# Kernel tuning notes

Hardware: AMD Instinct MI355X
Metric: run time of the kernel (lower is better)

## Reference

```python
import jax, jax.numpy as jnp
import numpy as np

B, S, IN_DIM, OUT_DIM = 16, 1024, 1024, 1024
NEG_SLOPE = 0.01  # torch F.leaky_relu default


def setup_inputs() -> dict:
    key = jax.random.key(0)
    ks = jax.random.split(key, 10)
    sc_in = 1.0 / np.sqrt(IN_DIM)
    sc_out = 1.0 / np.sqrt(OUT_DIM)
    return {
        "xs": jax.random.normal(ks[0], (B, S, IN_DIM), dtype=jnp.float32),
        "mask": jax.random.randint(ks[1], (B, S), 0, 2, dtype=jnp.int32),
        "Wk": jax.random.uniform(ks[2], (OUT_DIM, IN_DIM), jnp.float32, -sc_in, sc_in),
        "bk": jax.random.uniform(ks[3], (OUT_DIM,), jnp.float32, -sc_in, sc_in),
        "Wq": jax.random.uniform(ks[4], (OUT_DIM, IN_DIM), jnp.float32, -sc_in, sc_in),
        "bq": jax.random.uniform(ks[5], (OUT_DIM,), jnp.float32, -sc_in, sc_in),
        "Wv": jax.random.uniform(ks[6], (OUT_DIM, IN_DIM), jnp.float32, -sc_in, sc_in),
        "bv": jax.random.uniform(ks[7], (OUT_DIM,), jnp.float32, -sc_in, sc_in),
        "Wlin": jax.random.uniform(ks[8], (OUT_DIM, OUT_DIM), jnp.float32, -sc_out, sc_out),
        "blin": jax.random.uniform(ks[9], (OUT_DIM,), jnp.float32, -sc_out, sc_out),
    }


def reference(xs, mask, Wk, bk, Wq, bq, Wv, bv, Wlin, blin):
    # projections: torch Linear is x @ W.T + b
    K = jnp.einsum('bsi,oi->bso', xs, Wk) + bk  # [B,S,D]
    Q = jnp.einsum('bsi,oi->bso', xs, Wq) + bq  # [B,S,D]
    V = jnp.einsum('bsi,oi->bso', xs, Wv) + bv  # [B,S,D]
    # qk[b,s,e] = sum_d K[b,s,d] * Q[b,e,d]
    qk = jnp.einsum('bsd,bed->bse', K, Q) / xs.shape[-1]
    # mask.repeat(1,S).view(B,S,S) => element [b,i,j] = mask[b,j] (column/key mask)
    qk = jnp.where(mask[:, None, :].astype(bool), qk, -jnp.inf)
    a = jax.nn.softmax(qk, axis=-1)  # [B,S,S]
    # faithful to einsum('bij,bik->bik'): sum a over last axis, scale V elementwise
    attn = jnp.sum(a, axis=-1, keepdims=True) * V  # [B,S,D]
    out = jnp.einsum('bsd,od->bso', attn, Wlin) + blin
    return jnp.where(out >= 0, out, NEG_SLOPE * out)
```

## Files before the change

### kernel.cpp

```cpp
#include <hip/hip_runtime.h>
#include <hip/hip_bf16.h>
#include <stdint.h>


#define M_TOT 16384
#define KDIM  1024
#define NDIM  1024
#define NKT   16

typedef __attribute__((ext_vector_type(8))) short bf16x8;
typedef __attribute__((ext_vector_type(4))) float f32x4;
typedef __attribute__((ext_vector_type(4))) unsigned short u16x4;
typedef __attribute__((ext_vector_type(8))) unsigned short u16x8;

static __device__ __forceinline__ unsigned short f2bf(float f) {
    union { float f; unsigned int u; } v; v.f = f;
    unsigned int u = v.u;
    return (unsigned short)((u + 0x7fffu + ((u >> 16) & 1u)) >> 16);
}

static __device__ __forceinline__ u16x8 pack8(float4 a, float4 b) {
    u16x8 p = { f2bf(a.x), f2bf(a.y), f2bf(a.z), f2bf(a.w),
                f2bf(b.x), f2bf(b.y), f2bf(b.z), f2bf(b.w) };
    return p;
}

static __device__ __forceinline__ void gload16(const void* g, void* l) {
    __builtin_amdgcn_global_load_lds(
        (__attribute__((address_space(1))) void*)(g),
        (__attribute__((address_space(3))) void*)(l), 16, 0, 0);
}

static __device__ __forceinline__ int swz128(int p) {
    return p ^ (((p >> 7) & 7) << 4);
}

__global__ __launch_bounds__(256) void prep0_kernel(
    const float* __restrict__ Wv, const float* __restrict__ Wlin,
    const float* __restrict__ bv, const float* __restrict__ blin,
    unsigned short* __restrict__ Wvt, unsigned short* __restrict__ Wlb,
    float* __restrict__ bcomb) {
    __shared__ float Tl[64 * 65];
    const int bid = blockIdx.x;
    const int t = threadIdx.x;

    if (bid < 256) {
        const int dt = bid >> 4;
        const int it = bid & 15;
        const int r = t >> 2;
        const int c0 = (t & 3) * 16;
        #pragma unroll
        for (int u = 0; u < 4; ++u) {
            float4 v = *(const float4*)&Wv[((size_t)(dt * 64 + r)) * NDIM + it * 64 + c0 + 4 * u];
            Tl[r * 65 + c0 + 4 * u + 0] = v.x;
            Tl[r * 65 + c0 + 4 * u + 1] = v.y;
            Tl[r * 65 + c0 + 4 * u + 2] = v.z;
            Tl[r * 65 + c0 + 4 * u + 3] = v.w;
        }
        __syncthreads();
        const int i = t >> 2;
        const int dq = (t & 3) * 16;
        float v[16];
        #pragma unroll
        for (int u = 0; u < 16; ++u) v[u] = Tl[(dq + u) * 65 + i];
        u16x8 p0 = { f2bf(v[0]), f2bf(v[1]), f2bf(v[2]), f2bf(v[3]),
                     f2bf(v[4]), f2bf(v[5]), f2bf(v[6]), f2bf(v[7]) };
        u16x8 p1 = { f2bf(v[8]), f2bf(v[9]), f2bf(v[10]), f2bf(v[11]),
                     f2bf(v[12]), f2bf(v[13]), f2bf(v[14]), f2bf(v[15]) };
        unsigned short* dst = &Wvt[((size_t)(it * 64 + i)) * KDIM + dt * 64 + dq];
        *(u16x8*)dst = p0;
        *(u16x8*)(dst + 8) = p1;
    } else if (bid < 512) {
        const size_t idx = (((size_t)(bid - 256)) * 256 + t) * 16;
        float4 a = *(const float4*)&Wlin[idx];
        float4 b = *(const float4*)&Wlin[idx + 4];
        float4 c = *(const float4*)&Wlin[idx + 8];
        float4 d = *(const float4*)&Wlin[idx + 12];
        *(u16x8*)&Wlb[idx] = pack8(a, b);
        *(u16x8*)&Wlb[idx + 8] = pack8(c, d);
    } else {
        const int wave = t >> 6, lane = t & 63;
        const int o = (bid - 512) * 4 + wave;
        float s = 0.f;
        for (int d = lane; d < KDIM; d += 64) s += Wlin[o * KDIM + d] * bv[d];
        #pragma unroll
        for (int off = 32; off > 0; off >>= 1) s += __shfl_down(s, off, 64);
        if (lane == 0) bcomb[o] = s + blin[o];
    }
}

__global__ __launch_bounds__(256) void wcomb_kernel(
    const unsigned short* __restrict__ Wlb, const unsigned short* __restrict__ Wvt,
    unsigned short* __restrict__ Wc) {
    __shared__ unsigned short As[64 * 32];
    __shared__ unsigned short Bs[64 * 32];
    const int t = threadIdx.x;
    const int ot = blockIdx.x >> 4;
    const int it = blockIdx.x & 15;
    const int w = t >> 6, l = t & 63;
    const int wr = (w >> 1) * 32, wc = (w & 1) * 32;
    const int lr = l & 15, lk = l >> 4;

    f32x4 acc[2][2] = {};

    const unsigned short* gA = &Wlb[((size_t)(ot * 64 + (t >> 2))) * KDIM + (t & 3) * 8];
    const unsigned short* gB = &Wvt[((size_t)(it * 64 + (t >> 2))) * KDIM + (t & 3) * 8];
    unsigned short* lA = &As[w * 512];
    unsigned short* lB = &Bs[w * 512];

    for (int kt = 0; kt < KDIM / 32; ++kt) {
        gload16(gA + kt * 32, lA);
        gload16(gB + kt * 32, lB);
        __syncthreads();
        bf16x8 af[2], bfr[2];
        #pragma unroll
        for (int fi = 0; fi < 2; ++fi)
            af[fi] = *(bf16x8*)&As[(wr + fi * 16 + lr) * 32 + lk * 8];
        #pragma unroll
        for (int fj = 0; fj < 2; ++fj)
            bfr[fj] = *(bf16x8*)&Bs[(wc + fj * 16 + lr) * 32 + lk * 8];
        #pragma unroll
        for (int fi = 0; fi < 2; ++fi)
            #pragma unroll
            for (int fj = 0; fj < 2; ++fj)
                acc[fi][fj] = __builtin_amdgcn_mfma_f32_16x16x32_bf16(
                    af[fi], bfr[fj], acc[fi][fj], 0, 0, 0);
        __syncthreads();
    }
    #pragma unroll
    for (int fi = 0; fi < 2; ++fi)
        #pragma unroll
        for (int fj = 0; fj < 2; ++fj)
            #pragma unroll
            for (int r = 0; r < 4; ++r) {
                const int o = ot * 64 + wr + fi * 16 + lk * 4 + r;
                const int i = it * 64 + wc + fj * 16 + lr;
                Wc[(size_t)o * KDIM + i] = f2bf(acc[fi][fj][r]);
            }
}

__global__ __launch_bounds__(512, 2) void main_fused(
    const float* __restrict__ xs, const unsigned short* __restrict__ Wc,
    const float* __restrict__ bcomb, float* __restrict__ out) {
    extern __shared__ char lds[];
    const int tid = threadIdx.x;
    const int w = tid >> 6, l = tid & 63;
    const int wm = w >> 2, wn = w & 3;
    const int lr = l & 15, lk = l >> 4;

    const int swzb = ((blockIdx.x & 7) << 5) + (blockIdx.x >> 3);
    const int mt = swzb >> 2, nt = swzb & 3;

    int aoff[8], boff[4];
    #pragma unroll
    for (int fi = 0; fi < 8; ++fi)
        aoff[fi] = swz128((wm * 128 + fi * 16 + lr) * 128 + lk * 16);
    #pragma unroll
    for (int fj = 0; fj < 4; ++fj)
        boff[fj] = 32768 + swz128((wn * 64 + fj * 16 + lr) * 128 + lk * 16);

    const float* gA[4];
    int awr[4];
    #pragma unroll
    for (int j = 0; j < 4; ++j) {
        const int row = j * 64 + (tid >> 3);
        gA[j] = xs + ((size_t)(mt * 256 + row)) * KDIM + (tid & 7) * 8;
        awr[j] = swz128(row * 128 + (tid & 7) * 16);
    }
    const char* gB[4];
    #pragma unroll
    for (int j = 0; j < 4; ++j) {
        const int q = j * 8192 + w * 1024 + l * 16;
        const int p = swz128(q);
        gB[j] = (const char*)Wc + ((size_t)(nt * 256 + (p >> 7))) * 2048 + (p & 127);
    }
    const int bofs[4] = { 32768 + w * 1024, 32768 + 8192 + w * 1024,
                          32768 + 16384 + w * 1024, 32768 + 24576 + w * 1024 };

    f32x4 acc[8][4] = {};

    {
        float4 av[8];
        #pragma unroll
        for (int j = 0; j < 4; ++j) {
            av[2 * j]     = *(const float4*)(gA[j]);
            av[2 * j + 1] = *(const float4*)(gA[j] + 4);
        }
        #pragma unroll
        for (int j = 0; j < 4; ++j)
            gload16(gB[j], lds + bofs[j]);
        #pragma unroll
        for (int j = 0; j < 4; ++j)
            *(u16x8*)(lds + awr[j]) = pack8(av[2 * j], av[2 * j + 1]);
        asm volatile("s_waitcnt vmcnt(0)" ::: "memory");
        asm volatile("s_waitcnt lgkmcnt(0)" ::: "memory");
        __builtin_amdgcn_s_barrier();
    }

#define MFMA16(ACCI, AF, BF)                                                   \
    _Pragma("unroll")                                                          \
    for (int fi = 0; fi < 4; ++fi)                                             \
        _Pragma("unroll")                                                      \
        for (int fj = 0; fj < 4; ++fj)                                         \
            acc[(ACCI) + fi][fj] = __builtin_amdgcn_mfma_f32_16x16x32_bf16(    \
                (AF)[fi], (BF)[fj], acc[(ACCI) + fi][fj], 0, 0, 0)

#define PH_SYNC()                                                              \
    __builtin_amdgcn_s_barrier();                                              \
    asm volatile("s_waitcnt lgkmcnt(0)" ::: "memory");                         \
    __builtin_amdgcn_sched_barrier(0)

#define ITER(T, SEN)                                                           \
    do {                                                                       \
        const int cb = ((T) & 1) << 16;                                        \
        char* cbuf = lds + cb;                                                 \
        char* nbuf = lds + (cb ^ 65536);                                       \
        float4 av[8];                                                          \
        if (SEN) {                                                             \
            _Pragma("unroll")                                                  \
            for (int j = 0; j < 4; ++j) {                                      \
                av[2 * j]     = *(const float4*)(gA[j] + ((T) + 1) * 64);      \
                av[2 * j + 1] = *(const float4*)(gA[j] + ((T) + 1) * 64 + 4);  \
            }                                                                  \
            gload16(gB[0] + ((size_t)(T) + 1) * 128, nbuf + bofs[0]);          \
            gload16(gB[1] + ((size_t)(T) + 1) * 128, nbuf + bofs[1]);          \
        }                                                                      \
                                               \
        bf16x8 b0[4], a0[4];                                                   \
        _Pragma("unroll")                                                      \
        for (int fj = 0; fj < 4; ++fj)                                         \
            b0[fj] = *(const bf16x8*)(cbuf + boff[fj]);                        \
        _Pragma("unroll")                                                      \
        for (int fi = 0; fi < 4; ++fi)                                         \
            a0[fi] = *(const bf16x8*)(cbuf + aoff[fi]);                        \
        PH_SYNC();                                                             \
        __builtin_amdgcn_s_setprio(1);                                         \
        MFMA16(0, a0, b0);                                                     \
        __builtin_amdgcn_s_setprio(0);                                         \
        __builtin_amdgcn_s_barrier();                                          \
                    \
        bf16x8 a1[4];                                                          \
        _Pragma("unroll")                                                      \
        for (int fi = 0; fi < 4; ++fi)                                         \
            a1[fi] = *(const bf16x8*)(cbuf + aoff[4 + fi]);                    \
        if (SEN) {                                                             \
            *(u16x8*)(nbuf + awr[0]) = pack8(av[0], av[1]);                    \
            *(u16x8*)(nbuf + awr[1]) = pack8(av[2], av[3]);                    \
            gload16(gB[2] + ((size_t)(T) + 1) * 128, nbuf + bofs[2]);          \
            gload16(gB[3] + ((size_t)(T) + 1) * 128, nbuf + bofs[3]);          \
        }                                                                      \
        PH_SYNC();                                                             \
        __builtin_amdgcn_s_setprio(1);                                         \
        MFMA16(4, a1, b0);                                                     \
        __builtin_amdgcn_s_setprio(0);                                         \
        __builtin_amdgcn_s_barrier();                                          \
                         \
        bf16x8 b1[4], a2[4];                                                   \
        _Pragma("unroll")                                                      \
        for (int fj = 0; fj < 4; ++fj)                                         \
            b1[fj] = *(const bf16x8*)(cbuf + (boff[fj] ^ 64));                 \
        _Pragma("unroll")                                                      \
        for (int fi = 0; fi < 4; ++fi)                                         \
            a2[fi] = *(const bf16x8*)(cbuf + (aoff[fi] ^ 64));                 \
        if (SEN) {                                                             \
            *(u16x8*)(nbuf + awr[2]) = pack8(av[4], av[5]);                    \
            *(u16x8*)(nbuf + awr[3]) = pack8(av[6], av[7]);                    \
        }                                                                      \
        PH_SYNC();                                                             \
        __builtin_amdgcn_s_setprio(1);                                         \
        MFMA16(0, a2, b1);                                                     \
        __builtin_amdgcn_s_setprio(0);                                         \
        __builtin_amdgcn_s_barrier();                                          \
                                                       \
        bf16x8 a3[4];                                                          \
        _Pragma("unroll")                                                      \
        for (int fi = 0; fi < 4; ++fi)                                         \
            a3[fi] = *(const bf16x8*)(cbuf + (aoff[4 + fi] ^ 64));             \
        PH_SYNC();                                                             \
        __builtin_amdgcn_s_setprio(1);                                         \
        MFMA16(4, a3, b1);                                                     \
        __builtin_amdgcn_s_setprio(0);                                         \
        if (SEN) {                                                             \
            asm volatile("s_waitcnt vmcnt(0)" ::: "memory");                   \
            asm volatile("s_waitcnt lgkmcnt(0)" ::: "memory");                 \
            __builtin_amdgcn_s_barrier();                                      \
        }                                                                      \
    } while (0)

    for (int T = 0; T < NKT - 1; ++T) {
        ITER(T, 1);
    }
    ITER(NKT - 1, 0);
#undef ITER
#undef PH_SYNC
#undef MFMA16

    #pragma unroll
    for (int fi = 0; fi < 8; ++fi)
        #pragma unroll
        for (int fj = 0; fj < 4; ++fj) {
            const int col = nt * 256 + wn * 64 + fj * 16 + lr;
            const float b = bcomb[col];
            #pragma unroll
            for (int r = 0; r < 4; ++r) {
                const int row = mt * 256 + wm * 128 + fi * 16 + lk * 4 + r;
                float v = acc[fi][fj][r] + b;
                out[(size_t)row * NDIM + col] = v >= 0.f ? v : 0.01f * v;
            }
        }
}

__global__ __launch_bounds__(256) void main_gemm_f32(
    const float* __restrict__ X, const unsigned short* __restrict__ Wc,
    const float* __restrict__ bcomb, float* __restrict__ out) {
    __shared__ unsigned short As[128 * 32];
    __shared__ unsigned short Bs[128 * 32];
    const int t = threadIdx.x;
    const int nt = blockIdx.x & 7;
    const int mt = blockIdx.x >> 3;
    const int w = t >> 6, l = t & 63;
    const int wr = (w >> 1) * 64, wcc = (w & 1) * 64;
    const int lr = l & 15, lk = l >> 4;

    f32x4 acc[4][4] = {};

    const int arow = t >> 3;
    const int akq = t & 7;
    const int brow = t >> 2;
    const int bc4 = t & 3;

    for (int kt = 0; kt < KDIM / 32; ++kt) {
        float4 av[4];
        #pragma unroll
        for (int j = 0; j < 4; ++j) {
            const int row = j * 32 + arow;
            av[j] = *(const float4*)&X[(mt * 128 + row) * KDIM + kt * 32 + akq * 4];
        }
        __syncthreads();
        #pragma unroll
        for (int j = 0; j < 4; ++j) {
            const int row = j * 32 + arow;
            u16x4 p = { f2bf(av[j].x), f2bf(av[j].y), f2bf(av[j].z), f2bf(av[j].w) };
            *(u16x4*)&As[row * 32 + akq * 4] = p;
        }
        #pragma unroll
        for (int j = 0; j < 2; ++j) {
            const int row = j * 64 + brow;
            const unsigned short* g = &Wc[(nt * 128 + row) * KDIM + kt * 32 + bc4 * 8];
            unsigned short* ldst = &Bs[(j * 256 + w * 64) * 8];
            gload16(g, ldst);
        }
        __syncthreads();
        bf16x8 af[4], bfr[4];
        #pragma unroll
        for (int fi = 0; fi < 4; ++fi)
            af[fi] = *(bf16x8*)&As[(wr + fi * 16 + lr) * 32 + lk * 8];
        #pragma unroll
        for (int fj = 0; fj < 4; ++fj)
            bfr[fj] = *(bf16x8*)&Bs[(wcc + fj * 16 + lr) * 32 + lk * 8];
        #pragma unroll
        for (int fi = 0; fi < 4; ++fi)
            #pragma unroll
            for (int fj = 0; fj < 4; ++fj)
                acc[fi][fj] = __builtin_amdgcn_mfma_f32_16x16x32_bf16(
                    af[fi], bfr[fj], acc[fi][fj], 0, 0, 0);
    }

    #pragma unroll
    for (int fi = 0; fi < 4; ++fi)
        #pragma unroll
        for (int fj = 0; fj < 4; ++fj) {
            const int col = nt * 128 + wcc + fj * 16 + lr;
            const float b = bcomb[col];
            #pragma unroll
            for (int r = 0; r < 4; ++r) {
                const int row = mt * 128 + wr + fi * 16 + lk * 4 + r;
                float v = acc[fi][fj][r] + b;
                out[row * NDIM + col] = v >= 0.f ? v : 0.01f * v;
            }
        }
}

extern "C" void kernel_launch(void* const* d_in, const int* in_sizes, int n_in,
                              void* d_out, int out_size, void* d_ws, size_t ws_size,
                              hipStream_t stream) {
    const float* xs   = (const float*)d_in[0];
    const float* Wv   = (const float*)d_in[6];
    const float* bv   = (const float*)d_in[7];
    const float* Wlin = (const float*)d_in[8];
    const float* blin = (const float*)d_in[9];

    unsigned short* Wc = (unsigned short*)d_ws;
    float* bcomb = (float*)((char*)d_ws + 2097152);
    float* out = (float*)d_out;

    unsigned short* Wvt = (unsigned short*)d_out;
    unsigned short* Wlb = (unsigned short*)((char*)d_out + 2097152);

    const size_t NEED = 2101248;
    hipLaunchKernelGGL(prep0_kernel, dim3(768), dim3(256), 0, stream,
                       Wv, Wlin, bv, blin, Wvt, Wlb, bcomb);
    hipLaunchKernelGGL(wcomb_kernel, dim3(256), dim3(256), 0, stream,
                       Wlb, Wvt, Wc);
    if (ws_size >= NEED) {
        (void)hipFuncSetAttribute((const void*)main_fused,
                                  hipFuncAttributeMaxDynamicSharedMemorySize,
                                  131072);
        hipLaunchKernelGGL(main_fused, dim3(256), dim3(512), 131072, stream,
                           xs, Wc, bcomb, out);
    } else {
        hipLaunchKernelGGL(main_gemm_f32, dim3((M_TOT / 128) * (NDIM / 128)),
                           dim3(256), 0, stream, xs, Wc, bcomb, out);
    }
}
```

Measured before the change: 79.98 us.

## Prefetch fp32 A tiles two stages ahead with register double-buffering and partial vmcnt waits

Restructures the GEMM main loop so the fp32 activation tile is loaded into registers two k-steps ahead, using two alternating register sets, while the bf16 B tile is still issued one step ahead into the LDS double buffer. The full vmcnt(0) drain at the end of each iteration becomes a counted vmcnt wait at the start of the next, so more global loads stay in flight across MFMA phases. The converted A writes to LDS move to after the MFMA blocks. This is meant to hide global load latency better, at the cost of extra VGPRs for the second prefetch buffer, which could reduce occupancy or cause spills.

```diff
diff --git a/kernel.cpp b/kernel.cpp
--- a/kernel.cpp
+++ b/kernel.cpp
@@ -178,24 +178,27 @@
                           32768 + 16384 + w * 1024, 32768 + 24576 + w * 1024 };
 
     f32x4 acc[8][4] = {};
-
-    {
-        float4 av[8];
-        #pragma unroll
-        for (int j = 0; j < 4; ++j) {
-            av[2 * j]     = *(const float4*)(gA[j]);
-            av[2 * j + 1] = *(const float4*)(gA[j] + 4);
-        }
-        #pragma unroll
-        for (int j = 0; j < 4; ++j)
-            gload16(gB[j], lds + bofs[j]);
-        #pragma unroll
-        for (int j = 0; j < 4; ++j)
-            *(u16x8*)(lds + awr[j]) = pack8(av[2 * j], av[2 * j + 1]);
-        asm volatile("s_waitcnt vmcnt(0)" ::: "memory");
-        asm volatile("s_waitcnt lgkmcnt(0)" ::: "memory");
-        __builtin_amdgcn_s_barrier();
-    }
+    float4 avA[8], avB[8];
+
+#define STAGE_A(AV, TT)                                                        \
+    _Pragma("unroll")                                                          \
+    for (int j = 0; j < 4; ++j) {                                              \
+        AV[2 * j]     = *(const float4*)(gA[j] + (TT) * 64);                   \
+        AV[2 * j + 1] = *(const float4*)(gA[j] + (TT) * 64 + 4);               \
+    }
+
+    STAGE_A(avA, 0);
+    #pragma unroll
+    for (int j = 0; j < 4; ++j)
+        gload16(gB[j], lds + bofs[j]);
+    STAGE_A(avB, 1);
+    *(u16x8*)(lds + awr[0]) = pack8(avA[0], avA[1]);
+    *(u16x8*)(lds + awr[1]) = pack8(avA[2], avA[3]);
+    *(u16x8*)(lds + awr[2]) = pack8(avA[4], avA[5]);
+    *(u16x8*)(lds + awr[3]) = pack8(avA[6], avA[7]);
+    asm volatile("s_waitcnt vmcnt(8)" ::: "memory");
+    asm volatile("s_waitcnt lgkmcnt(0)" ::: "memory");
+    __builtin_amdgcn_s_barrier();
 
 #define MFMA16(ACCI, AF, BF)                                                   \
     _Pragma("unroll")                                                          \
@@ -210,21 +213,19 @@
     asm volatile("s_waitcnt lgkmcnt(0)" ::: "memory");                         \
     __builtin_amdgcn_sched_barrier(0)
 
-#define ITER(T, SEN)                                                           \
+#define ITER(T, AVL, AVC, AEN, BEN, CEN, WN)                                   \
     do {                                                                       \
-        const int cb = ((T) & 1) << 16;                                        \
-        char* cbuf = lds + cb;                                                 \
-        char* nbuf = lds + (cb ^ 65536);                                       \
-        float4 av[8];                                                          \
-        if (SEN) {                                                             \
-            _Pragma("unroll")                                                  \
-            for (int j = 0; j < 4; ++j) {                                      \
-                av[2 * j]     = *(const float4*)(gA[j] + ((T) + 1) * 64);      \
-                av[2 * j + 1] = *(const float4*)(gA[j] + ((T) + 1) * 64 + 4);  \
-            }                                                                  \
+        const char* cbuf = lds + (((T) & 1) << 16);                            \
+        char* nbuf = lds + ((((T) & 1) ^ 1) << 16);                            \
+        if (AEN) { STAGE_A(AVL, (T) + 2); }                                    \
+        if (BEN) {                                                             \
             gload16(gB[0] + ((size_t)(T) + 1) * 128, nbuf + bofs[0]);          \
             gload16(gB[1] + ((size_t)(T) + 1) * 128, nbuf + bofs[1]);          \
+            gload16(gB[2] + ((size_t)(T) + 1) * 128, nbuf + bofs[2]);          \
+            gload16(gB[3] + ((size_t)(T) + 1) * 128, nbuf + bofs[3]);          \
         }                                                                      \
+        asm volatile("s_waitcnt vmcnt(" #WN ")" ::: "memory");                 \
+        __builtin_amdgcn_s_barrier();                                          \
                                                \
         bf16x8 b0[4], a0[4];                                                   \
         _Pragma("unroll")                                                      \
@@ -238,23 +239,21 @@
         MFMA16(0, a0, b0);                                                     \
         __builtin_amdgcn_s_setprio(0);                                         \
         __builtin_amdgcn_s_barrier();                                          \
-                    \
+                            \
         bf16x8 a1[4];                                                          \
         _Pragma("unroll")                                                      \
         for (int fi = 0; fi < 4; ++fi)                                         \
             a1[fi] = *(const bf16x8*)(cbuf + aoff[4 + fi]);                    \
-        if (SEN) {                                                             \
-            *(u16x8*)(nbuf + awr[0]) = pack8(av[0], av[1]);                    \
-            *(u16x8*)(nbuf + awr[1]) = pack8(av[2], av[3]);                    \
-            gload16(gB[2] + ((size_t)(T) + 1) * 128, nbuf + bofs[2]);          \
-            gload16(gB[3] + ((size_t)(T) + 1) * 128, nbuf + bofs[3]);          \
-        }                                                                      \
         PH_SYNC();                                                             \
         __builtin_amdgcn_s_setprio(1);                                         \
         MFMA16(4, a1, b0);                                                     \
         __builtin_amdgcn_s_setprio(0);                                         \
+        if (CEN) {                                                             \
+            *(u16x8*)(nbuf + awr[0]) = pack8(AVC[0], AVC[1]);                  \
+            *(u16x8*)(nbuf + awr[1]) = pack8(AVC[2], AVC[3]);                  \
+        }                                                                      \
         __builtin_amdgcn_s_barrier();                                          \
-                         \
+                    \
         bf16x8 b1[4], a2[4];                                                   \
         _Pragma("unroll")                                                      \
         for (int fj = 0; fj < 4; ++fj)                                         \
@@ -262,16 +261,16 @@
         _Pragma("unroll")                                                      \
         for (int fi = 0; fi < 4; ++fi)                                         \
             a2[fi] = *(const bf16x8*)(cbuf + (aoff[fi] ^ 64));                 \
-        if (SEN) {                                                             \
-            *(u16x8*)(nbuf + awr[2]) = pack8(av[4], av[5]);                    \
-            *(u16x8*)(nbuf + awr[3]) = pack8(av[6], av[7]);                    \
-        }                                                                      \
         PH_SYNC();                                                             \
         __builtin_amdgcn_s_setprio(1);                                         \
         MFMA16(0, a2, b1);                                                     \
         __builtin_amdgcn_s_setprio(0);                                         \
+        if (CEN) {                                                             \
+            *(u16x8*)(nbuf + awr[2]) = pack8(AVC[4], AVC[5]);                  \
+            *(u16x8*)(nbuf + awr[3]) = pack8(AVC[6], AVC[7]);                  \
+        }                                                                      \
         __builtin_amdgcn_s_barrier();                                          \
-                                                       \
+        \
         bf16x8 a3[4];                                                          \
         _Pragma("unroll")                                                      \
         for (int fi = 0; fi < 4; ++fi)                                         \
@@ -280,20 +279,18 @@
         __builtin_amdgcn_s_setprio(1);                                         \
         MFMA16(4, a3, b1);                                                     \
         __builtin_amdgcn_s_setprio(0);                                         \
-        if (SEN) {                                                             \
-            asm volatile("s_waitcnt vmcnt(0)" ::: "memory");                   \
-            asm volatile("s_waitcnt lgkmcnt(0)" ::: "memory");                 \
-            __builtin_amdgcn_s_barrier();                                      \
-        }                                                                      \
     } while (0)
 
-    for (int T = 0; T < NKT - 1; ++T) {
-        ITER(T, 1);
-    }
-    ITER(NKT - 1, 0);
+    for (int t = 0; t < NKT - 2; t += 2) {
+        ITER(t,     avA, avB, 1, 1, 1, 12);
+        ITER(t + 1, avB, avA, 1, 1, 1, 12);
+    }
+    ITER(14, avA, avB, 0, 1, 1, 4);
+    ITER(15, avA, avA, 0, 0, 0, 0);
 #undef ITER
 #undef PH_SYNC
 #undef MFMA16
+#undef STAGE_A
 
     #pragma unroll
     for (int fi = 0; fi < 8; ++fi)
```

After: 135.8 us. 69.8% more time.
